# Optimization experiments

Hardware: AMD Instinct MI355X
Metric: run time of the kernel (lower is better)

Reference implementation:

```python
import jax, jax.numpy as jnp
import numpy as np

H = 500      # hidden size of RNNCell
D_IN = 512   # VGG16 feature channels
D_OUT = 100  # output vocab/logit dim
STEPS = 49   # 7x7 spatial grid consumed sequentially


def setup_inputs() -> dict:
    key = jax.random.key(0)
    ks = jax.random.split(key, 8)
    # post-VGG16 feature map for one 224x224 image: [1, 512, 7, 7]
    x = jax.random.normal(ks[0], (1, D_IN, 7, 7), dtype=jnp.float32)
    # original code uses torch.rand for the initial hidden state
    hidden0 = jax.random.uniform(ks[1], (1, H), dtype=jnp.float32)
    # nn.RNNCell(512, 500) params, PyTorch layout: W_ih [H, D_IN], W_hh [H, H]
    s_rnn = 1.0 / np.sqrt(H)
    W_ih = jax.random.uniform(ks[2], (H, D_IN), minval=-s_rnn, maxval=s_rnn, dtype=jnp.float32)
    W_hh = jax.random.uniform(ks[3], (H, H), minval=-s_rnn, maxval=s_rnn, dtype=jnp.float32)
    b_ih = jax.random.uniform(ks[4], (H,), minval=-s_rnn, maxval=s_rnn, dtype=jnp.float32)
    b_hh = jax.random.uniform(ks[5], (H,), minval=-s_rnn, maxval=s_rnn, dtype=jnp.float32)
    # nn.Linear(500, 100): W_out [D_OUT, H]
    s_out = 1.0 / np.sqrt(H)
    W_out = jax.random.uniform(ks[6], (D_OUT, H), minval=-s_out, maxval=s_out, dtype=jnp.float32)
    b_out = jax.random.uniform(ks[7], (D_OUT,), minval=-s_out, maxval=s_out, dtype=jnp.float32)
    return {"x": x, "hidden0": hidden0, "W_ih": W_ih, "W_hh": W_hh,
            "b_ih": b_ih, "b_hh": b_hh, "W_out": W_out, "b_out": b_out}


def reference(x, hidden0, W_ih, W_hh, b_ih, b_hh, W_out, b_out):
    # x: [1, 512, 7, 7] -> permute(0,2,3,1) -> [1,7,7,512] -> view(49, 1, 512)
    seq = jnp.transpose(x, (0, 2, 3, 1)).reshape(STEPS, 1, D_IN)
    # Precompute the input projection for all steps in one GEMM: [49, 1, H]
    xproj = jnp.einsum('tbd,hd->tbh', seq, W_ih) + b_ih + b_hh

    def step(h, xp):
        # h: [1, H]; RNNCell: h' = tanh(x W_ih^T + b_ih + h W_hh^T + b_hh)
        h = jnp.tanh(xp + h @ W_hh.T)
        out = jnp.tanh(h @ W_out.T + b_out)  # [1, D_OUT]
        return h, out

    _, outs = jax.lax.scan(step, hidden0, xproj)  # outs: [49, 1, 100]
    # torch.stack(op, 0).squeeze().unsqueeze(0) -> [1, 49, 100]
    return outs.squeeze(1)[None, :, :]
```

## Files before the change

kernel.cpp:

```cpp
#include <hip/hip_runtime.h>
#include <hip/hip_bf16.h>

#define H 500
#define D_IN 512
#define D_OUT 100
#define STEPS 49
#define NWG 4
#define RPW 125

typedef _Float16 h2_t __attribute__((ext_vector_type(2)));

#if defined(__has_builtin)
#if __has_builtin(__builtin_amdgcn_fdot2)
#define HAVE_FDOT2 1
#endif
#endif

__device__ __forceinline__ float fdot2f(h2_t a, h2_t b, float c) {
#ifdef HAVE_FDOT2
    return __builtin_amdgcn_fdot2(a, b, c, false);
#else
    return c + (float)a[0] * (float)b[0] + (float)a[1] * (float)b[1];
#endif
}
__device__ __forceinline__ h2_t bch2(unsigned u) { return __builtin_bit_cast(h2_t, u); }
__device__ __forceinline__ unsigned pk(float a, float b) {
    return __builtin_bit_cast(unsigned, h2_t{(_Float16)a, (_Float16)b});
}
__device__ __forceinline__ float tanh_fast(float x) {
    const float e = __expf(2.f * x);
    return 1.f - 2.f / (e + 1.f);
}

__global__ void k1_xproj(const float* __restrict__ x, const float* __restrict__ W_ih,
                         const float* __restrict__ b_ih, const float* __restrict__ b_hh,
                         float* __restrict__ xproj) {
    const int wv = threadIdx.x >> 6, lane = threadIdx.x & 63;
    const int r = blockIdx.x * 4 + wv;
    float wr[8];
#pragma unroll
    for (int k = 0; k < 8; k++) wr[k] = W_ih[r * D_IN + k * 64 + lane];
    float p[STEPS];
#pragma unroll
    for (int t = 0; t < STEPS; t++) p[t] = 0.f;
#pragma unroll
    for (int k = 0; k < 8; k++) {
        const float* xr = x + (size_t)(k * 64 + lane) * STEPS;
#pragma unroll
        for (int t = 0; t < STEPS; t++) p[t] = fmaf(wr[k], xr[t], p[t]);
    }
#pragma unroll
    for (int t = 0; t < STEPS; t++) {
        float v = p[t];
        v += __shfl_xor(v, 32); v += __shfl_xor(v, 16); v += __shfl_xor(v, 8);
        v += __shfl_xor(v, 4);  v += __shfl_xor(v, 2);  v += __shfl_xor(v, 1);
        p[t] = v;
    }
    if (lane == 0) {
        const float b = b_ih[r] + b_hh[r];
        for (int t = 0; t < STEPS; t++) xproj[t * 512 + r] = p[t] + b;
    }
}

__global__ void __launch_bounds__(512, 1)
k2_scan(const float* __restrict__ hidden0, const float* __restrict__ W_hh,
        const float* __restrict__ xproj, float* hbuf, float* __restrict__ Hs) {
    __shared__ uint4 wq[16][512];
    __shared__ _Float16 hlds[2][512];
    __shared__ float pbuf[NWG][128];

    const int g = blockIdx.x, tid = threadIdx.x;
    const int q = tid >> 7, r = tid & 127;
    const int row = g * RPW + r;

#pragma unroll
    for (int c = 0; c < 16; c++) {
        uint4 u = uint4{0u, 0u, 0u, 0u};
        if (r < RPW) {
            const float* rowp = W_hh + (size_t)row * H;
            const int c0 = 128 * q + 8 * c;
            if (c0 + 7 < H) {
                const float4 f0 = *(const float4*)(rowp + c0);
                const float4 f1 = *(const float4*)(rowp + c0 + 4);
                u.x = pk(f0.x, f0.y); u.y = pk(f0.z, f0.w);
                u.z = pk(f1.x, f1.y); u.w = pk(f1.z, f1.w);
            } else {
                float f[8];
#pragma unroll
                for (int e = 0; e < 8; e++) {
                    const int col = c0 + e;
                    f[e] = (col < H) ? rowp[col] : 0.f;
                }
                u.x = pk(f[0], f[1]); u.y = pk(f[2], f[3]);
                u.z = pk(f[4], f[5]); u.w = pk(f[6], f[7]);
            }
        }
        wq[c][tid] = u;
    }
    hlds[0][tid] = (tid < H) ? (_Float16)hidden0[tid] : (_Float16)0.f;
    hlds[1][tid] = (_Float16)0.f;
    __syncthreads();

#pragma unroll 1
    for (int t = 0; t < STEPS; ++t) {
        const int cur = t & 1, nxt = cur ^ 1;
        float xp = 0.f;
        if (q == 0 && r < RPW) xp = xproj[t * 512 + row];

        const uint4* hc = (const uint4*)&hlds[cur][0] + 16 * q;
        float s0 = 0.f, s1 = 0.f, s2 = 0.f, s3 = 0.f;
#pragma unroll
        for (int c = 0; c < 16; c++) {
            const uint4 wv_ = wq[c][tid];
            const uint4 hb = hc[c];
            s0 = fdot2f(bch2(wv_.x), bch2(hb.x), s0);
            s1 = fdot2f(bch2(wv_.y), bch2(hb.y), s1);
            s2 = fdot2f(bch2(wv_.z), bch2(hb.z), s2);
            s3 = fdot2f(bch2(wv_.w), bch2(hb.w), s3);
        }
        if (q != 0) pbuf[q][r] = (s0 + s1) + (s2 + s3);
        __syncthreads();

        if (q == 0 && r < RPW) {
            const float tot = (s0 + s1) + (s2 + s3)
                            + pbuf[1][r] + pbuf[2][r] + pbuf[3][r] + xp;
            const float hv = tanh_fast(tot);
            Hs[t * 512 + row] = hv;
            __hip_atomic_store(&hbuf[(t + 1) * 512 + row], hv,
                               __ATOMIC_RELAXED, __HIP_MEMORY_SCOPE_AGENT);
            hlds[nxt][row] = (_Float16)hv;
        }
        const bool own_word = (tid >= g * RPW) && (tid < g * RPW + RPW);
        if ((t + 1 < STEPS) && (tid < H) && !own_word) {
            unsigned* p = (unsigned*)&hbuf[(t + 1) * 512 + tid];
            unsigned bits_;
            do {
                bits_ = __hip_atomic_load(p, __ATOMIC_RELAXED, __HIP_MEMORY_SCOPE_AGENT);
            } while (bits_ == 0xFFFFFFFFu);
            hlds[nxt][tid] = (_Float16)__builtin_bit_cast(float, bits_);
        }
        __syncthreads();
    }
}

__global__ void k3_out(const float* __restrict__ Hs, const float* __restrict__ W_out,
                       const float* __restrict__ b_out, float* __restrict__ out) {
    const int t = blockIdx.x, o = threadIdx.x;
    if (o < D_OUT) {
        const float4* wr = (const float4*)(W_out + o * H);
        const float4* hr = (const float4*)(Hs + t * 512);
        float acc = b_out[o];
#pragma unroll 5
        for (int i = 0; i < 125; i++) {
            const float4 wv = wr[i];
            const float4 hv = hr[i];
            acc = fmaf(wv.x, hv.x, acc);
            acc = fmaf(wv.y, hv.y, acc);
            acc = fmaf(wv.z, hv.z, acc);
            acc = fmaf(wv.w, hv.w, acc);
        }
        out[t * D_OUT + o] = tanh_fast(acc);
    }
}

extern "C" void kernel_launch(void* const* d_in, const int* in_sizes, int n_in,
                              void* d_out, int out_size, void* d_ws, size_t ws_size,
                              hipStream_t stream) {
    const float* x       = (const float*)d_in[0];
    const float* hidden0 = (const float*)d_in[1];
    const float* W_ih    = (const float*)d_in[2];
    const float* W_hh    = (const float*)d_in[3];
    const float* b_ih    = (const float*)d_in[4];
    const float* b_hh    = (const float*)d_in[5];
    const float* W_out   = (const float*)d_in[6];
    const float* b_out   = (const float*)d_in[7];
    float* out = (float*)d_out;

    char* ws = (char*)d_ws;
    float* xproj = (float*)ws;
    float* Hs    = (float*)(ws + 100352);
    float* hbuf  = (float*)(ws + 200704);

    hipMemsetAsync(hbuf, 0xFF, 50 * 512 * 4, stream);
    k1_xproj<<<125, 256, 0, stream>>>(x, W_ih, b_ih, b_hh, xproj);
    k2_scan<<<NWG, 512, 0, stream>>>(hidden0, W_hh, xproj, hbuf, Hs);
    k3_out<<<STEPS, 128, 0, stream>>>(Hs, W_out, b_out, out);
}
```

Before: 108.6 us.

## Partition recurrent matvec by columns and exchange partial sums across workgroups

The recurrent scan switches from a row split to a column split. Each workgroup now owns a 128-wide chunk of the hidden state and computes partial dot products for all 500 rows against only that chunk. Partial sums for other workgroups' rows are published to global memory and the owner polls for them. This removes the broadcast of the full hidden vector to every workgroup and the extra intra-block reduction barrier. In exchange each step has three remote polls per row, a larger sentinel buffer to memset, and shuffle reductions.

Result: faster. 103.6 us (-4.6%).

```diff
diff --git a/kernel.cpp b/kernel.cpp
--- a/kernel.cpp
+++ b/kernel.cpp
@@ -6,7 +6,7 @@
 #define D_OUT 100
 #define STEPS 49
 #define NWG 4
-#define RPW 125
+#define SENT 0xFFFFFFFFu
 
 typedef _Float16 h2_t __attribute__((ext_vector_type(2)));
 
@@ -31,6 +31,7 @@
     const float e = __expf(2.f * x);
     return 1.f - 2.f / (e + 1.f);
 }
+__device__ __forceinline__ int clen(int g) { return (g < 3) ? 128 : (H - 384); }
 
 __global__ void k1_xproj(const float* __restrict__ x, const float* __restrict__ W_ih,
                          const float* __restrict__ b_ih, const float* __restrict__ b_hh,
@@ -64,80 +65,105 @@
 
 __global__ void __launch_bounds__(512, 1)
 k2_scan(const float* __restrict__ hidden0, const float* __restrict__ W_hh,
-        const float* __restrict__ xproj, float* hbuf, float* __restrict__ Hs) {
-    __shared__ uint4 wq[16][512];
-    __shared__ _Float16 hlds[2][512];
-    __shared__ float pbuf[NWG][128];
+        const float* __restrict__ xproj, float* part, float* __restrict__ Hs) {
+    __shared__ uint4 wl[16 * 512];
+    __shared__ __align__(16) _Float16 hch[2][128];
 
     const int g = blockIdx.x, tid = threadIdx.x;
-    const int q = tid >> 7, r = tid & 127;
-    const int row = g * RPW + r;
-
-#pragma unroll
-    for (int c = 0; c < 16; c++) {
-        uint4 u = uint4{0u, 0u, 0u, 0u};
-        if (r < RPW) {
-            const float* rowp = W_hh + (size_t)row * H;
-            const int c0 = 128 * q + 8 * c;
-            if (c0 + 7 < H) {
-                const float4 f0 = *(const float4*)(rowp + c0);
-                const float4 f1 = *(const float4*)(rowp + c0 + 4);
-                u.x = pk(f0.x, f0.y); u.y = pk(f0.z, f0.w);
-                u.z = pk(f1.x, f1.y); u.w = pk(f1.z, f1.w);
+    const int rr = tid >> 2, sub = tid & 3;
+    const int myLen = clen(g);
+
+#pragma unroll
+    for (int d = 0; d < 4; d++) {
+        uint4 u[4] = {{0,0,0,0},{0,0,0,0},{0,0,0,0},{0,0,0,0}};
+        if (rr < clen(d)) {
+            const int row = 128 * d + rr;
+            const float* rowp = W_hh + (size_t)row * H + 128 * g + 32 * sub;
+            const int cmax = myLen - 32 * sub;
+            if (cmax >= 32) {
+#pragma unroll
+                for (int q8 = 0; q8 < 4; q8++) {
+                    const float4 f0 = *(const float4*)(rowp + 8 * q8);
+                    const float4 f1 = *(const float4*)(rowp + 8 * q8 + 4);
+                    u[q8].x = pk(f0.x, f0.y); u[q8].y = pk(f0.z, f0.w);
+                    u[q8].z = pk(f1.x, f1.y); u[q8].w = pk(f1.z, f1.w);
+                }
             } else {
-                float f[8];
-#pragma unroll
-                for (int e = 0; e < 8; e++) {
-                    const int col = c0 + e;
-                    f[e] = (col < H) ? rowp[col] : 0.f;
+                float f[32];
+#pragma unroll
+                for (int cc = 0; cc < 32; cc++) f[cc] = (cc < cmax) ? rowp[cc] : 0.f;
+#pragma unroll
+                for (int q8 = 0; q8 < 4; q8++) {
+                    u[q8].x = pk(f[8*q8+0], f[8*q8+1]);
+                    u[q8].y = pk(f[8*q8+2], f[8*q8+3]);
+                    u[q8].z = pk(f[8*q8+4], f[8*q8+5]);
+                    u[q8].w = pk(f[8*q8+6], f[8*q8+7]);
                 }
-                u.x = pk(f[0], f[1]); u.y = pk(f[2], f[3]);
-                u.z = pk(f[4], f[5]); u.w = pk(f[6], f[7]);
             }
         }
-        wq[c][tid] = u;
-    }
-    hlds[0][tid] = (tid < H) ? (_Float16)hidden0[tid] : (_Float16)0.f;
-    hlds[1][tid] = (_Float16)0.f;
+#pragma unroll
+        for (int c = 0; c < 4; c++) wl[(d * 4 + c) * 512 + tid] = u[c];
+    }
+    if (tid < 128) hch[0][tid] = (tid < myLen) ? (_Float16)hidden0[128 * g + tid]
+                                               : (_Float16)0.f;
+    else if (tid < 256) hch[1][tid - 128] = (_Float16)0.f;
     __syncthreads();
 
 #pragma unroll 1
     for (int t = 0; t < STEPS; ++t) {
-        const int cur = t & 1, nxt = cur ^ 1;
+        const int cur = t & 1;
         float xp = 0.f;
-        if (q == 0 && r < RPW) xp = xproj[t * 512 + row];
-
-        const uint4* hc = (const uint4*)&hlds[cur][0] + 16 * q;
-        float s0 = 0.f, s1 = 0.f, s2 = 0.f, s3 = 0.f;
-#pragma unroll
-        for (int c = 0; c < 16; c++) {
-            const uint4 wv_ = wq[c][tid];
-            const uint4 hb = hc[c];
-            s0 = fdot2f(bch2(wv_.x), bch2(hb.x), s0);
-            s1 = fdot2f(bch2(wv_.y), bch2(hb.y), s1);
-            s2 = fdot2f(bch2(wv_.z), bch2(hb.z), s2);
-            s3 = fdot2f(bch2(wv_.w), bch2(hb.w), s3);
-        }
-        if (q != 0) pbuf[q][r] = (s0 + s1) + (s2 + s3);
-        __syncthreads();
-
-        if (q == 0 && r < RPW) {
-            const float tot = (s0 + s1) + (s2 + s3)
-                            + pbuf[1][r] + pbuf[2][r] + pbuf[3][r] + xp;
+        if (sub == 0 && rr < myLen) xp = xproj[t * 512 + 128 * g + rr];
+
+        const uint4* hc = (const uint4*)&hch[cur][0];
+        uint4 hv4[4];
+#pragma unroll
+        for (int c = 0; c < 4; c++) hv4[c] = hc[sub * 4 + c];
+
+        float own = 0.f;
+#pragma unroll
+        for (int k = 0; k < 4; k++) {
+            const int d = (g + 1 + k) & 3;
+            float s = 0.f;
+#pragma unroll
+            for (int c = 0; c < 4; c++) {
+                const uint4 w = wl[(d * 4 + c) * 512 + tid];
+                const uint4 hb = hv4[c];
+                s = fdot2f(bch2(w.x), bch2(hb.x), s);
+                s = fdot2f(bch2(w.y), bch2(hb.y), s);
+                s = fdot2f(bch2(w.z), bch2(hb.z), s);
+                s = fdot2f(bch2(w.w), bch2(hb.w), s);
+            }
+            s += __shfl_xor(s, 1);
+            s += __shfl_xor(s, 2);
+            if (k < 3) {
+                if (sub == 0)
+                    __hip_atomic_store(&part[((t * 4 + d) * 4 + g) * 128 + rr], s,
+                                       __ATOMIC_RELAXED, __HIP_MEMORY_SCOPE_AGENT);
+            } else own = s;
+        }
+
+        if (sub == 0 && rr < myLen) {
+            const int g1 = (g + 1) & 3, g2 = (g + 2) & 3, g3 = (g + 3) & 3;
+            const float* pb = &part[(t * 4 + g) * 4 * 128];
+            unsigned b1 = SENT, b2 = SENT, b3 = SENT;
+            do {
+                if (b1 == SENT) b1 = __builtin_bit_cast(unsigned,
+                    __hip_atomic_load(&pb[g1 * 128 + rr], __ATOMIC_RELAXED,
+                                      __HIP_MEMORY_SCOPE_AGENT));
+                if (b2 == SENT) b2 = __builtin_bit_cast(unsigned,
+                    __hip_atomic_load(&pb[g2 * 128 + rr], __ATOMIC_RELAXED,
+                                      __HIP_MEMORY_SCOPE_AGENT));
+                if (b3 == SENT) b3 = __builtin_bit_cast(unsigned,
+                    __hip_atomic_load(&pb[g3 * 128 + rr], __ATOMIC_RELAXED,
+                                      __HIP_MEMORY_SCOPE_AGENT));
+            } while (b1 == SENT || b2 == SENT || b3 == SENT);
+            const float tot = own + __builtin_bit_cast(float, b1)
+                                  + __builtin_bit_cast(float, b2)
+                                  + __builtin_bit_cast(float, b3) + xp;
             const float hv = tanh_fast(tot);
-            Hs[t * 512 + row] = hv;
-            __hip_atomic_store(&hbuf[(t + 1) * 512 + row], hv,
-                               __ATOMIC_RELAXED, __HIP_MEMORY_SCOPE_AGENT);
-            hlds[nxt][row] = (_Float16)hv;
-        }
-        const bool own_word = (tid >= g * RPW) && (tid < g * RPW + RPW);
-        if ((t + 1 < STEPS) && (tid < H) && !own_word) {
-            unsigned* p = (unsigned*)&hbuf[(t + 1) * 512 + tid];
-            unsigned bits_;
-            do {
-                bits_ = __hip_atomic_load(p, __ATOMIC_RELAXED, __HIP_MEMORY_SCOPE_AGENT);
-            } while (bits_ == 0xFFFFFFFFu);
-            hlds[nxt][tid] = (_Float16)__builtin_bit_cast(float, bits_);
+            Hs[t * 512 + 128 * g + rr] = hv;
+            hch[cur ^ 1][rr] = (_Float16)hv;
         }
         __syncthreads();
     }
@@ -177,12 +203,12 @@
     float* out = (float*)d_out;
 
     char* ws = (char*)d_ws;
-    float* xproj = (float*)ws;
-    float* Hs    = (float*)(ws + 100352);
-    float* hbuf  = (float*)(ws + 200704);
-
-    hipMemsetAsync(hbuf, 0xFF, 50 * 512 * 4, stream);
+    float* part  = (float*)ws;
+    float* xproj = (float*)(ws + 401408);
+    float* Hs    = (float*)(ws + 501760);
+
+    hipMemsetAsync(part, 0xFF, 401408, stream);
     k1_xproj<<<125, 256, 0, stream>>>(x, W_ih, b_ih, b_hh, xproj);
-    k2_scan<<<NWG, 512, 0, stream>>>(hidden0, W_hh, xproj, hbuf, Hs);
+    k2_scan<<<NWG, 512, 0, stream>>>(hidden0, W_hh, xproj, part, Hs);
     k3_out<<<STEPS, 128, 0, stream>>>(Hs, W_out, b_out, out);
 }
```
